# Kernel tuning notes

Measured on AMD Instinct MI355X. Metric: run time of the kernel, lower is better.

## Reference

```python
import jax, jax.numpy as jnp
import numpy as np

# nuScenes-scale config: batch 2, 360x360 BEV grid (1440/4), 128 channels,
# 10 classes, 200 proposals, 3x3 NMS kernel, 40k occupied voxels per sample.
B, H, W_GRID, NUM_CLS, NUM_PROP, NMS_K = 2, 360, 360, 10, 200, 3
C = 128
N_PER_B = 40000
NEG_FILL = -1000000.0  # scatter_nd fill value from to_dense()


def _bev_pos():
    # replicates create_2D_grid: coord = (x_index_along_dim1, y_index_along_dim0)
    xs = jnp.arange(H, dtype=jnp.float32)
    ys = jnp.arange(W_GRID, dtype=jnp.float32)
    by, bx = jnp.meshgrid(xs, ys, indexing='ij')  # by[i,j]=i, bx[i,j]=j
    return jnp.stack([bx, by], axis=-1).reshape(-1, 2)  # [H*W, 2]


def setup_inputs() -> dict:
    key = jax.random.key(0)
    ks = jax.random.split(key, 10)
    # unique spatial locations per batch sample (sparse voxel coords)
    flats = [jax.random.permutation(ks[i], H * W_GRID)[:N_PER_B] for i in range(B)]
    flat = jnp.concatenate(flats)
    b = jnp.repeat(jnp.arange(B), N_PER_B)
    indices = jnp.stack([b, flat // W_GRID, flat % W_GRID], axis=1).astype(jnp.int32)
    features = jax.random.normal(ks[4], (B * N_PER_B, C), jnp.float32)
    # heatmap head (pointwise linears standing in for the submconv stack)
    W_hm1 = jax.random.normal(ks[5], (C, C), jnp.float32) * (2.0 / C) ** 0.5
    b_hm1 = jnp.zeros((C,), jnp.float32)
    W_hm2 = jax.random.normal(ks[6], (C, NUM_CLS), jnp.float32) * (2.0 / C) ** 0.5
    b_hm2 = jnp.full((NUM_CLS,), -2.19, jnp.float32)  # fc[-1].bias.fill_(-2.19)
    # class_encoding: nn.Conv1d(num_class, channels, 1)
    W_cls = jax.random.normal(ks[7], (C, NUM_CLS), jnp.float32) * 0.1
    b_cls = jnp.zeros((C,), jnp.float32)
    return dict(features=features, W_hm1=W_hm1, b_hm1=b_hm1, W_hm2=W_hm2,
                b_hm2=b_hm2, W_cls=W_cls, b_cls=b_cls, indices=indices)


def reference(features, W_hm1, b_hm1, W_hm2, b_hm2, W_cls, b_cls, indices):
    bidx, yi, xi = indices[:, 0], indices[:, 1], indices[:, 2]
    HW = H * W_GRID

    # --- x.dense(): scatter voxel features to dense BEV grid (zero fill) ---
    xd = jnp.zeros((B, H, W_GRID, C), features.dtype).at[bidx, yi, xi].set(features)
    x_flat = xd.reshape(B, HW, C).transpose(0, 2, 1)  # [B, C, HW]

    # --- heatmap head (per-voxel) then to_dense() with -1e6 fill ---
    hm = jax.nn.relu(features @ W_hm1 + b_hm1) @ W_hm2 + b_hm2  # [N, NUM_CLS]
    dense_hm = jnp.full((B, H, W_GRID, NUM_CLS), NEG_FILL, hm.dtype)
    dense_hm = dense_hm.at[bidx, yi, xi].set(hm).transpose(0, 3, 1, 2)  # [B,K,H,W]

    heat = jax.nn.sigmoid(dense_hm)  # detached in original

    # --- NMS-kernel peak extraction ---
    pad = NMS_K // 2
    inner = jax.lax.reduce_window(heat, -jnp.inf, jax.lax.max,
                                  (1, 1, NMS_K, NMS_K), (1, 1, 1, 1), 'VALID')
    local_max = jnp.zeros_like(heat).at[:, :, pad:H - pad, pad:W_GRID - pad].set(inner)
    # pedestrian (8) and traffic_cone (9): kernel size 1
    local_max = local_max.at[:, 8].set(heat[:, 8]).at[:, 9].set(heat[:, 9])
    heat = heat * (heat == local_max)
    heat_f = heat.reshape(B, NUM_CLS, HW)

    # --- top-k proposals over (class, location) ---
    _, top = jax.lax.top_k(heat_f.reshape(B, -1), NUM_PROP)  # [B, P]
    cls = top // HW
    idx = top % HW

    # --- gather proposal features + class encoding ---
    qf = jnp.take_along_axis(x_flat, jnp.broadcast_to(idx[:, None, :], (B, C, NUM_PROP)), axis=2)
    onehot = jax.nn.one_hot(cls, NUM_CLS, dtype=qf.dtype)  # [B, P, K]
    qf = qf + jnp.einsum('ck,bpk->bcp', W_cls, onehot) + b_cls[None, :, None]

    # --- proposal positions and heatmap scores ---
    query_pos = _bev_pos()[idx]  # [B, P, 2]
    qhs = jnp.take_along_axis(heat_f, jnp.broadcast_to(idx[:, None, :], (B, NUM_CLS, NUM_PROP)), axis=2)
    return qf, query_pos, qhs, cls
```

## Files before the change

kernel.cpp:

```cpp
#include <hip/hip_runtime.h>

#define HW 129600
#define WG 360
#define HG 360
#define NCLS 10
#define NPROP 200
#define CDIM 128
#define NROWS 80000
#define NB 2
#define SEL_CAP 8192
#define HBINS 4096
#define CHUNK 4096
#define RPB 64
#define FSTRIDE 132

__device__ __forceinline__ float nms_val(const float* __restrict__ hp, int pos,
                                         int cl) {
  float v = hp[pos];
  if (cl >= 8) return v;
  int y = pos / WG, x = pos - y * WG;
  if (y == 0 || y == HG - 1 || x == 0 || x == WG - 1) return 0.f;
  float m = v;
  m = fmaxf(m, hp[pos - 1]);
  m = fmaxf(m, hp[pos + 1]);
  m = fmaxf(m, hp[pos - WG - 1]);
  m = fmaxf(m, hp[pos - WG]);
  m = fmaxf(m, hp[pos - WG + 1]);
  m = fmaxf(m, hp[pos + WG - 1]);
  m = fmaxf(m, hp[pos + WG]);
  m = fmaxf(m, hp[pos + WG + 1]);
  return (v == m) ? v : 0.f;
}

__global__ __launch_bounds__(256) void k_head(
    const float* __restrict__ feat, const float* __restrict__ W1,
    const float* __restrict__ b1, const float* __restrict__ W2,
    const float* __restrict__ b2, const int* __restrict__ idxs,
    float* __restrict__ dense_heat, int* __restrict__ rowmap) {
  __shared__ __align__(16) float lds_f[RPB * FSTRIDE];
  __shared__ int lds_b[RPB];
  __shared__ int lds_p[RPB];
  const int tid = threadIdx.x;
  const int row0 = blockIdx.x * RPB;

  if (tid < RPB) {
    int row = row0 + tid;
    int bb = idxs[row * 3 + 0];
    int yy = idxs[row * 3 + 1];
    int xx = idxs[row * 3 + 2];
    lds_b[tid] = bb;
    lds_p[tid] = yy * WG + xx;
    rowmap[(size_t)bb * HW + yy * WG + xx] = row;
  }
#pragma unroll
  for (int i = 0; i < 8; ++i) {
    int fi = tid + i * 256;
    int r = fi >> 5, k4 = fi & 31;
    float4 v = *(const float4*)(feat + (size_t)(row0 + r) * CDIM + k4 * 4);
    *(float4*)(lds_f + r * FSTRIDE + k4 * 4) = v;
  }
  __syncthreads();

  const int lane = tid & 63;
  const int c0 = __builtin_amdgcn_readfirstlane((tid >> 6) << 5);
  float acc[32];
#pragma unroll
  for (int c = 0; c < 32; ++c) acc[c] = 0.f;

  const float* fr = lds_f + lane * FSTRIDE;
  for (int k = 0; k < CDIM; k += 4) {
    float4 f4 = *(const float4*)(fr + k);
#pragma unroll
    for (int h = 0; h < 2; ++h) {
#pragma unroll
      for (int cc = 0; cc < 16; ++cc) {
        const int c = c0 + h * 16 + cc;
        float a = acc[h * 16 + cc];
        a = fmaf(f4.x, W1[(k + 0) * CDIM + c], a);
        a = fmaf(f4.y, W1[(k + 1) * CDIM + c], a);
        a = fmaf(f4.z, W1[(k + 2) * CDIM + c], a);
        a = fmaf(f4.w, W1[(k + 3) * CDIM + c], a);
        acc[h * 16 + cc] = a;
      }
    }
  }

  float p[NCLS];
#pragma unroll
  for (int j = 0; j < NCLS; ++j) p[j] = 0.f;
#pragma unroll
  for (int cc = 0; cc < 32; ++cc) {
    const int c = c0 + cc;
    float hv = fmaxf(acc[cc] + b1[c], 0.f);
#pragma unroll
    for (int j = 0; j < NCLS; ++j) p[j] = fmaf(hv, W2[c * NCLS + j], p[j]);
  }

  __syncthreads();
  float* part = lds_f;
  {
    const int w = tid >> 6;
#pragma unroll
    for (int j = 0; j < NCLS; ++j) part[w * (RPB * NCLS) + lane * NCLS + j] = p[j];
  }
  __syncthreads();
  for (int o = tid; o < RPB * NCLS; o += 256) {
    int r = o / NCLS, j = o - r * NCLS;
    float s = part[o] + part[640 + o] + part[1280 + o] + part[1920 + o] + b2[j];
    float heat = 1.0f / (1.0f + expf(-s));
    dense_heat[((size_t)lds_b[r] * NCLS + j) * HW + lds_p[r]] = heat;
  }
}

__global__ __launch_bounds__(256) void k_nms_hist(
    const float* __restrict__ dense_heat, unsigned int* __restrict__ hist) {
  __shared__ unsigned int lh[HBINS];
  const int cl = blockIdx.y;
  const int b = blockIdx.z;
  const int p0 = blockIdx.x * CHUNK;
  for (int i = threadIdx.x; i < HBINS; i += 256) lh[i] = 0;
  __syncthreads();
  const float* hp = dense_heat + ((size_t)b * NCLS + cl) * HW;
  for (int it = 0; it < CHUNK; it += 256) {
    int pos = p0 + it + threadIdx.x;
    if (pos < HW) {
      float out = nms_val(hp, pos, cl);
      if (out > 0.f) atomicAdd(&lh[__float_as_uint(out) >> 18], 1u);
    }
  }
  __syncthreads();
  unsigned int* gh = hist + (size_t)b * HBINS;
  for (int i = threadIdx.x; i < HBINS; i += 256) {
    unsigned int c = lh[i];
    if (c) atomicAdd(&gh[i], c);
  }
}

__global__ __launch_bounds__(256) void k_collect(
    const float* __restrict__ dense_heat, const unsigned int* __restrict__ hist,
    unsigned long long* __restrict__ sel, int* __restrict__ sel_cnt) {
  __shared__ unsigned int coarse[256];
  __shared__ int sT;
  const int cl = blockIdx.y;
  const int b = blockIdx.z;
  const unsigned int* h = hist + (size_t)b * HBINS;
  unsigned int s = 0;
  for (int i = 0; i < 16; ++i) s += h[threadIdx.x * 16 + i];
  coarse[threadIdx.x] = s;
  __syncthreads();
  if (threadIdx.x == 0) {
    unsigned int cum = 0;
    int T = 0;
    int ci = 255;
    for (; ci >= 0; --ci) {
      if (cum + coarse[ci] >= NPROP) break;
      cum += coarse[ci];
    }
    if (ci >= 0) {
      int t = 15;
      for (; t > 0; --t) {
        unsigned int c = h[ci * 16 + t];
        if (cum + c >= NPROP) break;
        cum += c;
      }
      T = ci * 16 + t;
    }
    sT = T;
  }
  __syncthreads();
  const int T = sT;
  const float* hp = dense_heat + ((size_t)b * NCLS + cl) * HW;
  const int p0 = blockIdx.x * CHUNK;
  for (int it = 0; it < CHUNK; it += 256) {
    int pos = p0 + it + threadIdx.x;
    float out = 0.f;
    if (pos < HW) out = nms_val(hp, pos, cl);
    unsigned int bits = __float_as_uint(out);
    bool pred = (out > 0.f) && ((int)(bits >> 18) >= T);
    unsigned long long mask = __ballot(pred);
    if (pred) {
      int lane = threadIdx.x & 63;
      int lb = __popcll(mask & ((1ull << lane) - 1ull));
      int base = 0;
      if (lb == 0) base = atomicAdd(&sel_cnt[b], (int)__popcll(mask));
      base = __builtin_amdgcn_readfirstlane(base);
      unsigned int gidx = (unsigned int)cl * HW + (unsigned int)pos;
      unsigned long long key =
          ((unsigned long long)bits << 32) | (unsigned long long)(~gidx);
      int slot = base + lb;
      if (slot < SEL_CAP) sel[(size_t)b * SEL_CAP + slot] = key;
    }
  }
}

__global__ __launch_bounds__(256) void k_final(
    const unsigned long long* __restrict__ sel, const int* __restrict__ sel_cnt,
    const float* __restrict__ dense_heat, const int* __restrict__ rowmap,
    const float* __restrict__ feat, const float* __restrict__ Wc,
    const float* __restrict__ bc, float* __restrict__ out) {
  __shared__ unsigned long long sk[SEL_CAP];
  __shared__ unsigned long long winners[NPROP];
  __shared__ int wpos[NPROP];
  __shared__ int wcls[NPROP];
  __shared__ int wrow[NPROP];
  const int b = blockIdx.x;
  const int tid = threadIdx.x;
  int M = sel_cnt[b];
  if (M > SEL_CAP) M = SEL_CAP;
  for (int i = tid; i < M; i += 256) sk[i] = sel[(size_t)b * SEL_CAP + i];
  __syncthreads();
  for (int i = tid; i < M; i += 256) {
    unsigned long long key = sk[i];
    int rank = 0;
    for (int j = 0; j < M; ++j) rank += (sk[j] > key) ? 1 : 0;
    if (rank < NPROP) winners[rank] = key;
  }
  __syncthreads();
  if (tid < NPROP) {
    unsigned long long key = winners[tid];
    unsigned int gidx = ~((unsigned int)(key & 0xFFFFFFFFull));
    int cls = (int)(gidx / HW);
    int pos = (int)(gidx - (unsigned int)cls * HW);
    int y = pos / WG, x = pos - y * WG;
    wpos[tid] = pos;
    wcls[tid] = cls;
    wrow[tid] = rowmap[(size_t)b * HW + pos];
    out[51200 + ((size_t)b * NPROP + tid) * 2 + 0] = (float)x;
    out[51200 + ((size_t)b * NPROP + tid) * 2 + 1] = (float)y;
    out[56000 + b * NPROP + tid] = (float)cls;
  }
  __syncthreads();
  for (int o = tid; o < NCLS * NPROP; o += 256) {
    int j = o / NPROP, pp = o - j * NPROP;
    const float* hp = dense_heat + ((size_t)b * NCLS + j) * HW;
    out[52000 + (size_t)b * NCLS * NPROP + o] = nms_val(hp, wpos[pp], j);
  }
  for (int o = tid; o < CDIM * NPROP; o += 256) {
    int c = o / NPROP, pp = o - c * NPROP;
    out[(size_t)b * CDIM * NPROP + o] =
        feat[(size_t)wrow[pp] * CDIM + c] + Wc[c * NCLS + wcls[pp]] + bc[c];
  }
}

extern "C" void kernel_launch(void* const* d_in, const int* in_sizes, int n_in,
                              void* d_out, int out_size, void* d_ws,
                              size_t ws_size, hipStream_t stream) {
  const float* feat = (const float*)d_in[0];
  const float* W1 = (const float*)d_in[1];
  const float* b1 = (const float*)d_in[2];
  const float* W2 = (const float*)d_in[3];
  const float* b2 = (const float*)d_in[4];
  const float* Wc = (const float*)d_in[5];
  const float* bc = (const float*)d_in[6];
  const int* idxs = (const int*)d_in[7];
  float* out = (float*)d_out;

  char* ws = (char*)d_ws;
  float* dense_heat = (float*)(ws + 0);
  unsigned int* hist = (unsigned int*)(ws + 10368000);
  int* rowmap = (int*)(ws + 10400768);
  unsigned long long* sel = (unsigned long long*)(ws + 11437568);
  int* sel_cnt = (int*)(ws + 11568640);

  hipMemsetAsync(dense_heat, 0, (size_t)NB * NCLS * HW * sizeof(float), stream);
  hipMemsetAsync(hist, 0, (size_t)NB * HBINS * sizeof(unsigned int), stream);
  hipMemsetAsync(sel_cnt, 0, 2 * sizeof(int), stream);

  k_head<<<NROWS / RPB, 256, 0, stream>>>(feat, W1, b1, W2, b2, idxs, dense_heat,
                                          rowmap);
  k_nms_hist<<<dim3((HW + CHUNK - 1) / CHUNK, NCLS, NB), 256, 0, stream>>>(
      dense_heat, hist);
  k_collect<<<dim3((HW + CHUNK - 1) / CHUNK, NCLS, NB), 256, 0, stream>>>(
      dense_heat, hist, sel, sel_cnt);
  k_final<<<NB, 256, 0, stream>>>(sel, sel_cnt, dense_heat, rowmap, feat, Wc, bc,
                                  out);
}
```

Measured before the change: 209.5 us.

## Retile head GEMM in LDS and fuse NMS/select/final into cooperative kernel

The head kernel now stages W1 and feature tiles in LDS with register prefetch and computes an 8x4 register-blocked outer product, then does the second linear layer from LDS with a transposed W2. The NMS histogram, threshold collection and final top-k/gather stages are merged into a single cooperative kernel with grid-wide syncs. That kernel keeps NMS values in registers, so the heat map is read once instead of twice, and two launches are removed. It adds a dependence on cooperative launch (1024 blocks must be co-resident) and shrinks SEL_CAP to 2048, which could overflow if many candidates pass the threshold.

```diff
diff --git a/kernel.cpp b/kernel.cpp
--- a/kernel.cpp
+++ b/kernel.cpp
@@ -1,4 +1,7 @@
 #include <hip/hip_runtime.h>
+#include <hip/hip_cooperative_groups.h>
+
+namespace cg = cooperative_groups;
 
 #define HW 129600
 #define WG 360
@@ -8,11 +11,13 @@
 #define CDIM 128
 #define NROWS 80000
 #define NB 2
-#define SEL_CAP 8192
+#define SEL_CAP 2048
 #define HBINS 4096
-#define CHUNK 4096
 #define RPB 64
-#define FSTRIDE 132
+#define TOTAL (NB * NCLS * HW)
+#define BH (NCLS * HW)
+#define SBLK 1024
+#define SPT 10
 
 __device__ __forceinline__ float nms_val(const float* __restrict__ hp, int pos,
                                          int cl) {
@@ -37,12 +42,20 @@
     const float* __restrict__ b1, const float* __restrict__ W2,
     const float* __restrict__ b2, const int* __restrict__ idxs,
     float* __restrict__ dense_heat, int* __restrict__ rowmap) {
-  __shared__ __align__(16) float lds_f[RPB * FSTRIDE];
+  __shared__ __align__(16) float lds_w[32 * 128];
+  __shared__ __align__(16) float lds_f[RPB * 32];
+  __shared__ __align__(16) float lds_w2t[NCLS * 128];
   __shared__ int lds_b[RPB];
   __shared__ int lds_p[RPB];
   const int tid = threadIdx.x;
   const int row0 = blockIdx.x * RPB;
-
+  const int tc = tid & 31;
+  const int tr = tid >> 5;
+
+  for (int i = tid; i < CDIM * NCLS; i += 256) {
+    int k = i / NCLS, j = i - k * NCLS;
+    lds_w2t[j * 128 + k] = W2[i];
+  }
   if (tid < RPB) {
     int row = row0 + tid;
     int bb = idxs[row * 3 + 0];
@@ -53,158 +66,222 @@
     rowmap[(size_t)bb * HW + yy * WG + xx] = row;
   }
 #pragma unroll
-  for (int i = 0; i < 8; ++i) {
-    int fi = tid + i * 256;
-    int r = fi >> 5, k4 = fi & 31;
-    float4 v = *(const float4*)(feat + (size_t)(row0 + r) * CDIM + k4 * 4);
-    *(float4*)(lds_f + r * FSTRIDE + k4 * 4) = v;
-  }
-  __syncthreads();
-
-  const int lane = tid & 63;
-  const int c0 = __builtin_amdgcn_readfirstlane((tid >> 6) << 5);
-  float acc[32];
-#pragma unroll
-  for (int c = 0; c < 32; ++c) acc[c] = 0.f;
-
-  const float* fr = lds_f + lane * FSTRIDE;
-  for (int k = 0; k < CDIM; k += 4) {
-    float4 f4 = *(const float4*)(fr + k);
-#pragma unroll
-    for (int h = 0; h < 2; ++h) {
-#pragma unroll
-      for (int cc = 0; cc < 16; ++cc) {
-        const int c = c0 + h * 16 + cc;
-        float a = acc[h * 16 + cc];
-        a = fmaf(f4.x, W1[(k + 0) * CDIM + c], a);
-        a = fmaf(f4.y, W1[(k + 1) * CDIM + c], a);
-        a = fmaf(f4.z, W1[(k + 2) * CDIM + c], a);
-        a = fmaf(f4.w, W1[(k + 3) * CDIM + c], a);
-        acc[h * 16 + cc] = a;
-      }
-    }
-  }
-
-  float p[NCLS];
-#pragma unroll
-  for (int j = 0; j < NCLS; ++j) p[j] = 0.f;
-#pragma unroll
-  for (int cc = 0; cc < 32; ++cc) {
-    const int c = c0 + cc;
-    float hv = fmaxf(acc[cc] + b1[c], 0.f);
-#pragma unroll
-    for (int j = 0; j < NCLS; ++j) p[j] = fmaf(hv, W2[c * NCLS + j], p[j]);
-  }
-
-  __syncthreads();
-  float* part = lds_f;
+  for (int q = 0; q < 4; ++q) {
+    int fi = tid + q * 256;
+    *(float4*)(lds_w + fi * 4) = *(const float4*)(W1 + fi * 4);
+  }
+#pragma unroll
+  for (int q = 0; q < 2; ++q) {
+    int fi = tid + q * 256;
+    int r = fi >> 3, kk = fi & 7;
+    *(float4*)(lds_f + r * 32 + kk * 4) =
+        *(const float4*)(feat + (size_t)(row0 + r) * CDIM + kk * 4);
+  }
+  __syncthreads();
+
+  float acc[8][4];
+#pragma unroll
+  for (int r = 0; r < 8; ++r)
+#pragma unroll
+    for (int c = 0; c < 4; ++c) acc[r][c] = 0.f;
+
+  for (int kt = 0; kt < 4; ++kt) {
+    float4 pw[4], pf[2];
+    if (kt < 3) {
+#pragma unroll
+      for (int q = 0; q < 4; ++q)
+        pw[q] = *(const float4*)(W1 + (kt + 1) * 4096 + (tid + q * 256) * 4);
+#pragma unroll
+      for (int q = 0; q < 2; ++q) {
+        int fi = tid + q * 256;
+        int r = fi >> 3, kk = fi & 7;
+        pf[q] = *(const float4*)(feat + (size_t)(row0 + r) * CDIM +
+                                 (kt + 1) * 32 + kk * 4);
+      }
+    }
+#pragma unroll
+    for (int kg = 0; kg < 8; ++kg) {
+      float4 w0 = *(const float4*)(lds_w + (kg * 4 + 0) * 128 + tc * 4);
+      float4 w1 = *(const float4*)(lds_w + (kg * 4 + 1) * 128 + tc * 4);
+      float4 w2 = *(const float4*)(lds_w + (kg * 4 + 2) * 128 + tc * 4);
+      float4 w3 = *(const float4*)(lds_w + (kg * 4 + 3) * 128 + tc * 4);
+#pragma unroll
+      for (int r = 0; r < 8; ++r) {
+        float4 fv = *(const float4*)(lds_f + (tr * 8 + r) * 32 + kg * 4);
+        acc[r][0] = fmaf(fv.x, w0.x, acc[r][0]);
+        acc[r][0] = fmaf(fv.y, w1.x, acc[r][0]);
+        acc[r][0] = fmaf(fv.z, w2.x, acc[r][0]);
+        acc[r][0] = fmaf(fv.w, w3.x, acc[r][0]);
+        acc[r][1] = fmaf(fv.x, w0.y, acc[r][1]);
+        acc[r][1] = fmaf(fv.y, w1.y, acc[r][1]);
+        acc[r][1] = fmaf(fv.z, w2.y, acc[r][1]);
+        acc[r][1] = fmaf(fv.w, w3.y, acc[r][1]);
+        acc[r][2] = fmaf(fv.x, w0.z, acc[r][2]);
+        acc[r][2] = fmaf(fv.y, w1.z, acc[r][2]);
+        acc[r][2] = fmaf(fv.z, w2.z, acc[r][2]);
+        acc[r][2] = fmaf(fv.w, w3.z, acc[r][2]);
+        acc[r][3] = fmaf(fv.x, w0.w, acc[r][3]);
+        acc[r][3] = fmaf(fv.y, w1.w, acc[r][3]);
+        acc[r][3] = fmaf(fv.z, w2.w, acc[r][3]);
+        acc[r][3] = fmaf(fv.w, w3.w, acc[r][3]);
+      }
+    }
+    __syncthreads();
+    if (kt < 3) {
+#pragma unroll
+      for (int q = 0; q < 4; ++q) *(float4*)(lds_w + (tid + q * 256) * 4) = pw[q];
+#pragma unroll
+      for (int q = 0; q < 2; ++q) {
+        int fi = tid + q * 256;
+        int r = fi >> 3, kk = fi & 7;
+        *(float4*)(lds_f + r * 32 + kk * 4) = pf[q];
+      }
+    }
+    __syncthreads();
+  }
+
+  float4 b1v = *(const float4*)(b1 + tc * 4);
+#pragma unroll
+  for (int half = 0; half < 2; ++half) {
+    if ((tr >> 2) == half) {
+      int ltr = tr & 3;
+#pragma unroll
+      for (int r = 0; r < 8; ++r) {
+        float4 h;
+        h.x = fmaxf(acc[r][0] + b1v.x, 0.f);
+        h.y = fmaxf(acc[r][1] + b1v.y, 0.f);
+        h.z = fmaxf(acc[r][2] + b1v.z, 0.f);
+        h.w = fmaxf(acc[r][3] + b1v.w, 0.f);
+        *(float4*)(lds_w + (ltr * 8 + r) * 128 + tc * 4) = h;
+      }
+    }
+    __syncthreads();
+    for (int o = tid; o < 32 * NCLS; o += 256) {
+      int r = o / NCLS, j = o - r * NCLS;
+      float s = b2[j];
+      for (int i4 = 0; i4 < 32; ++i4) {
+        int k4 = (i4 + tid) & 31;
+        float4 hv = *(const float4*)(lds_w + r * 128 + k4 * 4);
+        float4 wv = *(const float4*)(lds_w2t + j * 128 + k4 * 4);
+        s = fmaf(hv.x, wv.x, s);
+        s = fmaf(hv.y, wv.y, s);
+        s = fmaf(hv.z, wv.z, s);
+        s = fmaf(hv.w, wv.w, s);
+      }
+      float heat = 1.0f / (1.0f + expf(-s));
+      int gr = half * 32 + r;
+      dense_heat[((size_t)lds_b[gr] * NCLS + j) * HW + lds_p[gr]] = heat;
+    }
+    __syncthreads();
+  }
+}
+
+__global__ __launch_bounds__(256) void k_select(
+    const float* __restrict__ dense_heat, unsigned int* __restrict__ hist,
+    unsigned long long* __restrict__ sel, int* __restrict__ sel_cnt,
+    const int* __restrict__ rowmap, const float* __restrict__ feat,
+    const float* __restrict__ Wc, const float* __restrict__ bc,
+    float* __restrict__ out) {
+  __shared__ __align__(16) unsigned long long sk[SEL_CAP];
+  __shared__ int sT[2];
+  __shared__ unsigned long long winners[NPROP];
+  __shared__ int wpos[NPROP];
+  __shared__ int wcls[NPROP];
+  __shared__ int wrow[NPROP];
+  unsigned int* lh = (unsigned int*)sk;
+  cg::grid_group grid = cg::this_grid();
+  const int tid = threadIdx.x;
+  const int gbase = blockIdx.x * (256 * SPT);
+  const int blk_b = (gbase < BH) ? 0 : 1;
+
+  for (int i = tid; i < HBINS; i += 256) lh[i] = 0;
+  __syncthreads();
+  float val[SPT];
+#pragma unroll
+  for (int it = 0; it < SPT; ++it) {
+    int g = gbase + it * 256 + tid;
+    float v = 0.f;
+    if (g < TOTAL) {
+      int b = (g >= BH) ? 1 : 0;
+      int r = g - b * BH;
+      int cl = r / HW;
+      int pos = r - cl * HW;
+      v = nms_val(dense_heat + (size_t)(g - pos), pos, cl);
+      if (v > 0.f) {
+        unsigned int bin = __float_as_uint(v) >> 18;
+        if (b == blk_b)
+          atomicAdd(&lh[bin], 1u);
+        else
+          atomicAdd(&hist[(size_t)b * HBINS + bin], 1u);
+      }
+    }
+    val[it] = v;
+  }
+  __syncthreads();
   {
-    const int w = tid >> 6;
-#pragma unroll
-    for (int j = 0; j < NCLS; ++j) part[w * (RPB * NCLS) + lane * NCLS + j] = p[j];
-  }
-  __syncthreads();
-  for (int o = tid; o < RPB * NCLS; o += 256) {
-    int r = o / NCLS, j = o - r * NCLS;
-    float s = part[o] + part[640 + o] + part[1280 + o] + part[1920 + o] + b2[j];
-    float heat = 1.0f / (1.0f + expf(-s));
-    dense_heat[((size_t)lds_b[r] * NCLS + j) * HW + lds_p[r]] = heat;
-  }
-}
-
-__global__ __launch_bounds__(256) void k_nms_hist(
-    const float* __restrict__ dense_heat, unsigned int* __restrict__ hist) {
-  __shared__ unsigned int lh[HBINS];
-  const int cl = blockIdx.y;
-  const int b = blockIdx.z;
-  const int p0 = blockIdx.x * CHUNK;
-  for (int i = threadIdx.x; i < HBINS; i += 256) lh[i] = 0;
-  __syncthreads();
-  const float* hp = dense_heat + ((size_t)b * NCLS + cl) * HW;
-  for (int it = 0; it < CHUNK; it += 256) {
-    int pos = p0 + it + threadIdx.x;
-    if (pos < HW) {
-      float out = nms_val(hp, pos, cl);
-      if (out > 0.f) atomicAdd(&lh[__float_as_uint(out) >> 18], 1u);
-    }
-  }
-  __syncthreads();
-  unsigned int* gh = hist + (size_t)b * HBINS;
-  for (int i = threadIdx.x; i < HBINS; i += 256) {
-    unsigned int c = lh[i];
-    if (c) atomicAdd(&gh[i], c);
-  }
-}
-
-__global__ __launch_bounds__(256) void k_collect(
-    const float* __restrict__ dense_heat, const unsigned int* __restrict__ hist,
-    unsigned long long* __restrict__ sel, int* __restrict__ sel_cnt) {
-  __shared__ unsigned int coarse[256];
-  __shared__ int sT;
-  const int cl = blockIdx.y;
-  const int b = blockIdx.z;
-  const unsigned int* h = hist + (size_t)b * HBINS;
-  unsigned int s = 0;
-  for (int i = 0; i < 16; ++i) s += h[threadIdx.x * 16 + i];
-  coarse[threadIdx.x] = s;
-  __syncthreads();
-  if (threadIdx.x == 0) {
-    unsigned int cum = 0;
-    int T = 0;
-    int ci = 255;
-    for (; ci >= 0; --ci) {
-      if (cum + coarse[ci] >= NPROP) break;
-      cum += coarse[ci];
-    }
-    if (ci >= 0) {
-      int t = 15;
-      for (; t > 0; --t) {
-        unsigned int c = h[ci * 16 + t];
-        if (cum + c >= NPROP) break;
-        cum += c;
-      }
-      T = ci * 16 + t;
-    }
-    sT = T;
-  }
-  __syncthreads();
-  const int T = sT;
-  const float* hp = dense_heat + ((size_t)b * NCLS + cl) * HW;
-  const int p0 = blockIdx.x * CHUNK;
-  for (int it = 0; it < CHUNK; it += 256) {
-    int pos = p0 + it + threadIdx.x;
-    float out = 0.f;
-    if (pos < HW) out = nms_val(hp, pos, cl);
-    unsigned int bits = __float_as_uint(out);
-    bool pred = (out > 0.f) && ((int)(bits >> 18) >= T);
+    unsigned int* gh = hist + (size_t)blk_b * HBINS;
+    for (int i = tid; i < HBINS; i += 256) {
+      unsigned int c = lh[i];
+      if (c) atomicAdd(&gh[i], c);
+    }
+  }
+  grid.sync();
+
+  for (int bb = 0; bb < NB; ++bb) {
+    const unsigned int* h = hist + (size_t)bb * HBINS;
+    unsigned int s = 0;
+#pragma unroll
+    for (int i = 0; i < HBINS / 256; ++i) s += h[tid * (HBINS / 256) + i];
+    __syncthreads();
+    lh[tid] = s;
+    __syncthreads();
+    if (tid == 0) {
+      unsigned int cum = 0;
+      int T = 0;
+      int ci = 255;
+      for (; ci >= 0; --ci) {
+        if (cum + lh[ci] >= NPROP) break;
+        cum += lh[ci];
+      }
+      if (ci >= 0) {
+        int t = 15;
+        for (; t > 0; --t) {
+          unsigned int c = h[ci * 16 + t];
+          if (cum + c >= NPROP) break;
+          cum += c;
+        }
+        T = ci * 16 + t;
+      }
+      sT[bb] = T;
+    }
+    __syncthreads();
+  }
+  const int T0 = sT[0], T1 = sT[1];
+#pragma unroll
+  for (int it = 0; it < SPT; ++it) {
+    int g = gbase + it * 256 + tid;
+    float v = (g < TOTAL) ? val[it] : 0.f;
+    int b = (g >= BH) ? 1 : 0;
+    unsigned int bits = __float_as_uint(v);
+    bool pred = (v > 0.f) && ((int)(bits >> 18) >= (b ? T1 : T0));
     unsigned long long mask = __ballot(pred);
     if (pred) {
-      int lane = threadIdx.x & 63;
+      int lane = tid & 63;
       int lb = __popcll(mask & ((1ull << lane) - 1ull));
       int base = 0;
       if (lb == 0) base = atomicAdd(&sel_cnt[b], (int)__popcll(mask));
       base = __builtin_amdgcn_readfirstlane(base);
-      unsigned int gidx = (unsigned int)cl * HW + (unsigned int)pos;
+      unsigned int gidx = (unsigned int)(g - b * BH);
       unsigned long long key =
           ((unsigned long long)bits << 32) | (unsigned long long)(~gidx);
       int slot = base + lb;
       if (slot < SEL_CAP) sel[(size_t)b * SEL_CAP + slot] = key;
     }
   }
-}
-
-__global__ __launch_bounds__(256) void k_final(
-    const unsigned long long* __restrict__ sel, const int* __restrict__ sel_cnt,
-    const float* __restrict__ dense_heat, const int* __restrict__ rowmap,
-    const float* __restrict__ feat, const float* __restrict__ Wc,
-    const float* __restrict__ bc, float* __restrict__ out) {
-  __shared__ unsigned long long sk[SEL_CAP];
-  __shared__ unsigned long long winners[NPROP];
-  __shared__ int wpos[NPROP];
-  __shared__ int wcls[NPROP];
-  __shared__ int wrow[NPROP];
+  grid.sync();
+
   const int b = blockIdx.x;
-  const int tid = threadIdx.x;
+  if (b >= NB) return;
   int M = sel_cnt[b];
   if (M > SEL_CAP) M = SEL_CAP;
   for (int i = tid; i < M; i += 256) sk[i] = sel[(size_t)b * SEL_CAP + i];
@@ -260,7 +337,7 @@
   unsigned int* hist = (unsigned int*)(ws + 10368000);
   int* rowmap = (int*)(ws + 10400768);
   unsigned long long* sel = (unsigned long long*)(ws + 11437568);
-  int* sel_cnt = (int*)(ws + 11568640);
+  int* sel_cnt = (int*)(ws + 11470336);
 
   hipMemsetAsync(dense_heat, 0, (size_t)NB * NCLS * HW * sizeof(float), stream);
   hipMemsetAsync(hist, 0, (size_t)NB * HBINS * sizeof(unsigned int), stream);
@@ -268,10 +345,9 @@
 
   k_head<<<NROWS / RPB, 256, 0, stream>>>(feat, W1, b1, W2, b2, idxs, dense_heat,
                                           rowmap);
-  k_nms_hist<<<dim3((HW + CHUNK - 1) / CHUNK, NCLS, NB), 256, 0, stream>>>(
-      dense_heat, hist);
-  k_collect<<<dim3((HW + CHUNK - 1) / CHUNK, NCLS, NB), 256, 0, stream>>>(
-      dense_heat, hist, sel, sel_cnt);
-  k_final<<<NB, 256, 0, stream>>>(sel, sel_cnt, dense_heat, rowmap, feat, Wc, bc,
-                                  out);
+  void* args[] = {(void*)&dense_heat, (void*)&hist,   (void*)&sel,
+                  (void*)&sel_cnt,    (void*)&rowmap, (void*)&feat,
+                  (void*)&Wc,         (void*)&bc,     (void*)&out};
+  hipLaunchCooperativeKernel((const void*)k_select, dim3(SBLK), dim3(256), args,
+                             0, stream);
 }
```

Result: slower. 484.1 us (+131.1%).
